# Kernel tuning notes

Hardware: AMD Instinct MI355X
Metric: run time of the kernel (lower is better)

Reference implementation:

```python
import jax, jax.numpy as jnp
import numpy as np

KS = 3        # kernel_size
DIL = 2       # dilation
HEAD_DIM = 32


def _unfold(x, ks, dil):
    """torch nn.Unfold(ks, dilation=dil, padding=dil*(ks-1)//2, stride=1).
    x: [B, C, H, W] -> [B, C, ks*ks, H, W] (channel-major patch order, matching torch)."""
    B, C, H, W = x.shape
    pad = dil * (ks - 1) // 2
    xp = jnp.pad(x, ((0, 0), (0, 0), (pad, pad), (pad, pad)))
    pats = [xp[:, :, i * dil:i * dil + H, j * dil:j * dil + W]
            for i in range(ks) for j in range(ks)]
    return jnp.stack(pats, axis=2)


def setup_inputs() -> dict:
    key = jax.random.key(0)
    k1, k2, k3 = jax.random.split(key, 3)
    shape = (16, 128, 64, 64)  # [B, d, H, W]
    return {
        "q": jax.random.normal(k1, shape, dtype=jnp.float32),
        "k": jax.random.normal(k2, shape, dtype=jnp.float32),
        "v": jax.random.normal(k3, shape, dtype=jnp.float32),
    }


def reference(q, k, v):
    B, d, H, W = q.shape
    heads = d // HEAD_DIM
    scale = HEAD_DIM ** (-0.5)
    KK = KS * KS
    # q: [B, heads, head_dim, H*W]
    qr = q.reshape(B, heads, HEAD_DIM, H * W)
    # unfolded k/v: [B, heads, head_dim, KK, H*W]
    ku = _unfold(k, KS, DIL).reshape(B, heads, HEAD_DIM, KK, H * W)
    vu = _unfold(v, KS, DIL).reshape(B, heads, HEAD_DIM, KK, H * W)
    # per-pixel small attention over KK local dilated keys
    attn = jnp.einsum('bhdn,bhdkn->bhnk', qr, ku) * scale  # [B,heads,HW,KK]
    attn = jax.nn.softmax(attn, axis=-1)  # attn_drop = 0 -> identity
    out = jnp.einsum('bhnk,bhdkn->bnhd', attn, vu)  # [B,HW,heads,head_dim]
    return out.reshape(B, H, W, d)
```

## Files before the change

### kernel.cpp

```cpp
#include <hip/hip_runtime.h>

namespace {
constexpr float SCALE = 0.17677669529663687f;
constexpr int CHP = 256;

typedef const __attribute__((address_space(1))) void gbl_v;
typedef __attribute__((address_space(3))) void lds_v;
typedef float v2f __attribute__((ext_vector_type(2)));

__global__ __launch_bounds__(512, 4) void dilate_attn(
    const float* __restrict__ q, const float* __restrict__ k,
    const float* __restrict__ v, float* __restrict__ out) {
  __shared__ float kbuf[32 * CHP];
  __shared__ float vbuf[32 * CHP];

  const int tid = threadIdx.x;
  const int cg  = tid & 7;
  const int pp  = (tid >> 3) & 31;
  const int rg  = tid >> 8;

  const int blk   = blockIdx.x;
  const int s     = blk >> 3;
  const int combo = ((blk & 7) << 3) | (s >> 5);
  const int pr    = s & 31;
  const int r0    = ((pr >> 1) << 2) | (pr & 1);
  const int b     = combo >> 2;
  const int head  = combo & 3;
  const int qrow  = r0 + 2 * rg;

  const size_t cb = ((size_t)b * 128 + head * 32) * 4096;
  const float* kp = k + cb;
  const float* vp = v + cb;

  int srow[4]; float vm[4];
  #pragma unroll
  for (int j = 0; j < 4; ++j) {
    const int ry = r0 - 2 + 2 * j;
    const bool ok = (unsigned)ry < 64u;
    srow[j] = (ok ? ry : r0) * 64;
    vm[j]   = ok ? 1.0f : 0.0f;
  }

  const int px0 = pp << 1;
  v2f q2[4];
  #pragma unroll
  for (int ci = 0; ci < 4; ++ci) {
    q2[ci] = *(const v2f*)(q + cb + (cg * 4 + ci) * 4096 + qrow * 64 + px0);
    q2[ci] *= SCALE;
  }

  int goff[4], loff[4];
  #pragma unroll
  for (int t = 0; t < 4; ++t) {
    const int l4  = t * 512 + tid;
    const int ch  = l4 >> 6;
    const int rem = l4 & 63;
    const int r   = rem >> 4;
    const int q4  = rem & 15;
    const int pxs = ((q4 - (ch >> 2)) & 15) << 2;
    goff[t] = ch * 4096 + srow[r] + pxs;
    loff[t] = l4 << 2;
  }
  #pragma unroll
  for (int t = 0; t < 4; ++t)
    __builtin_amdgcn_global_load_lds((gbl_v*)(kp + goff[t]), (lds_v*)(kbuf + loff[t]), 16, 0, 0);
  #pragma unroll
  for (int t = 0; t < 4; ++t)
    __builtin_amdgcn_global_load_lds((gbl_v*)(vp + goff[t]), (lds_v*)(vbuf + loff[t]), 16, 0, 0);

  asm volatile("s_waitcnt vmcnt(4)" ::: "memory");
  __builtin_amdgcn_s_barrier();
  asm volatile("" ::: "memory");

  const int   txL = (pp == 0)  ? 0  : px0 - 2;
  const int   txC = px0;
  const int   txR = (pp == 31) ? 62 : px0 + 2;
  const float mL  = (pp == 0)  ? 0.0f : 1.0f;
  const float mR  = (pp == 31) ? 0.0f : 1.0f;

  const int rot = cg << 2;
  const int tL  = (txL + rot) & 63;
  const int tC  = (txC + rot) & 63;
  const int tR  = (txR + rot) & 63;

  const int rbase = rg;

  v2f l[9];
  #pragma unroll
  for (int t = 0; t < 9; ++t) l[t] = (v2f)(0.0f);

  #pragma unroll
  for (int r = 0; r < 3; ++r) {
    #pragma unroll
    for (int ci = 0; ci < 4; ++ci) {
      const float* kc = kbuf + (cg * 4 + ci) * CHP + (rbase + r) * 64;
      const v2f kL = *(const v2f*)(kc + tL);
      const v2f kC = *(const v2f*)(kc + tC);
      const v2f kR = *(const v2f*)(kc + tR);
      l[r*3+0] = __builtin_elementwise_fma(q2[ci], kL, l[r*3+0]);
      l[r*3+1] = __builtin_elementwise_fma(q2[ci], kC, l[r*3+1]);
      l[r*3+2] = __builtin_elementwise_fma(q2[ci], kR, l[r*3+2]);
    }
  }

  #pragma unroll
  for (int m = 1; m <= 4; m <<= 1) {
    #pragma unroll
    for (int t = 0; t < 9; ++t) {
      v2f tmp;
      tmp.x = __shfl_xor(l[t].x, m, 64);
      tmp.y = __shfl_xor(l[t].y, m, 64);
      l[t] += tmp;
    }
  }

  float msk[9];
  #pragma unroll
  for (int r = 0; r < 3; ++r) {
    msk[r*3+0] = vm[rbase + r] * mL;
    msk[r*3+1] = vm[rbase + r];
    msk[r*3+2] = vm[rbase + r] * mR;
  }
  v2f sum = (v2f)(0.0f);
  #pragma unroll
  for (int t = 0; t < 9; ++t) {
    l[t] *= msk[t];
    l[t].x = __expf(l[t].x);
    l[t].y = __expf(l[t].y);
    sum += l[t];
  }
  v2f rv; rv.x = 1.0f / sum.x; rv.y = 1.0f / sum.y;
  #pragma unroll
  for (int t = 0; t < 9; ++t)
    l[t] *= rv * msk[t];

  asm volatile("s_waitcnt vmcnt(0)" ::: "memory");
  __builtin_amdgcn_s_barrier();
  asm volatile("" ::: "memory");

  v2f o[4];
  #pragma unroll
  for (int ci = 0; ci < 4; ++ci) o[ci] = (v2f)(0.0f);
  #pragma unroll
  for (int r = 0; r < 3; ++r) {
    #pragma unroll
    for (int ci = 0; ci < 4; ++ci) {
      const float* vc = vbuf + (cg * 4 + ci) * CHP + (rbase + r) * 64;
      const v2f vL = *(const v2f*)(vc + tL);
      const v2f vC = *(const v2f*)(vc + tC);
      const v2f vR = *(const v2f*)(vc + tR);
      o[ci] = __builtin_elementwise_fma(l[r*3+0], vL, o[ci]);
      o[ci] = __builtin_elementwise_fma(l[r*3+1], vC, o[ci]);
      o[ci] = __builtin_elementwise_fma(l[r*3+2], vR, o[ci]);
    }
  }

  float* ob = out + ((size_t)(b * 64 + qrow) * 64 + px0) * 128 + head * 32 + cg * 4;
  *(float4*)(ob)       = make_float4(o[0].x, o[1].x, o[2].x, o[3].x);
  *(float4*)(ob + 128) = make_float4(o[0].y, o[1].y, o[2].y, o[3].y);
}
}

extern "C" void kernel_launch(void* const* d_in, const int* in_sizes, int n_in,
                              void* d_out, int out_size, void* d_ws, size_t ws_size,
                              hipStream_t stream) {
  const float* q = (const float*)d_in[0];
  const float* k = (const float*)d_in[1];
  const float* v = (const float*)d_in[2];
  float* o = (float*)d_out;
  dilate_attn<<<dim3(2048), dim3(512), 0, stream>>>(q, k, v, o);
}
```

Before: 140.2 us.

## Share one LDS buffer for K then V and use DPP for reductions

Replaces the separate K and V LDS buffers with a single 32 KB buffer. K is loaded and consumed first, then V is loaded into the same space after a barrier, which halves LDS per block and raises the launch-bounds occupancy target from 4 to 8. The first two butterfly steps of the channel reduction now use quad-permute DPP moves instead of ds_bpermute shuffles. In exchange, the V load no longer overlaps the QK and softmax computation and is fully serialized, and the extra __syncthreads calls add barrier overhead.

```diff
diff --git a/kernel.cpp b/kernel.cpp
--- a/kernel.cpp
+++ b/kernel.cpp
@@ -8,11 +8,16 @@
 typedef __attribute__((address_space(3))) void lds_v;
 typedef float v2f __attribute__((ext_vector_type(2)));
 
-__global__ __launch_bounds__(512, 4) void dilate_attn(
+template<int CTRL>
+__device__ __forceinline__ float qperm(float v) {
+  return __builtin_bit_cast(float, __builtin_amdgcn_mov_dpp(
+      __builtin_bit_cast(int, v), CTRL, 0xF, 0xF, true));
+}
+
+__global__ __launch_bounds__(512, 8) void dilate_attn(
     const float* __restrict__ q, const float* __restrict__ k,
     const float* __restrict__ v, float* __restrict__ out) {
-  __shared__ float kbuf[32 * CHP];
-  __shared__ float vbuf[32 * CHP];
+  __shared__ float sbuf[32 * CHP];
 
   const int tid = threadIdx.x;
   const int cg  = tid & 7;
@@ -61,16 +66,11 @@
     goff[t] = ch * 4096 + srow[r] + pxs;
     loff[t] = l4 << 2;
   }
+
   #pragma unroll
   for (int t = 0; t < 4; ++t)
-    __builtin_amdgcn_global_load_lds((gbl_v*)(kp + goff[t]), (lds_v*)(kbuf + loff[t]), 16, 0, 0);
-  #pragma unroll
-  for (int t = 0; t < 4; ++t)
-    __builtin_amdgcn_global_load_lds((gbl_v*)(vp + goff[t]), (lds_v*)(vbuf + loff[t]), 16, 0, 0);
-
-  asm volatile("s_waitcnt vmcnt(4)" ::: "memory");
-  __builtin_amdgcn_s_barrier();
-  asm volatile("" ::: "memory");
+    __builtin_amdgcn_global_load_lds((gbl_v*)(kp + goff[t]), (lds_v*)(sbuf + loff[t]), 16, 0, 0);
+  __syncthreads();
 
   const int   txL = (pp == 0)  ? 0  : px0 - 2;
   const int   txC = px0;
@@ -93,7 +93,7 @@
   for (int r = 0; r < 3; ++r) {
     #pragma unroll
     for (int ci = 0; ci < 4; ++ci) {
-      const float* kc = kbuf + (cg * 4 + ci) * CHP + (rbase + r) * 64;
+      const float* kc = sbuf + (cg * 4 + ci) * CHP + (rbase + r) * 64;
       const v2f kL = *(const v2f*)(kc + tL);
       const v2f kC = *(const v2f*)(kc + tC);
       const v2f kR = *(const v2f*)(kc + tR);
@@ -104,14 +104,19 @@
   }
 
   #pragma unroll
-  for (int m = 1; m <= 4; m <<= 1) {
-    #pragma unroll
-    for (int t = 0; t < 9; ++t) {
-      v2f tmp;
-      tmp.x = __shfl_xor(l[t].x, m, 64);
-      tmp.y = __shfl_xor(l[t].y, m, 64);
-      l[t] += tmp;
-    }
+  for (int t = 0; t < 9; ++t) {
+    l[t].x += qperm<0xB1>(l[t].x);
+    l[t].y += qperm<0xB1>(l[t].y);
+  }
+  #pragma unroll
+  for (int t = 0; t < 9; ++t) {
+    l[t].x += qperm<0x4E>(l[t].x);
+    l[t].y += qperm<0x4E>(l[t].y);
+  }
+  #pragma unroll
+  for (int t = 0; t < 9; ++t) {
+    l[t].x += __shfl_xor(l[t].x, 4, 64);
+    l[t].y += __shfl_xor(l[t].y, 4, 64);
   }
 
   float msk[9];
@@ -134,9 +139,11 @@
   for (int t = 0; t < 9; ++t)
     l[t] *= rv * msk[t];
 
-  asm volatile("s_waitcnt vmcnt(0)" ::: "memory");
-  __builtin_amdgcn_s_barrier();
-  asm volatile("" ::: "memory");
+  __syncthreads();
+  #pragma unroll
+  for (int t = 0; t < 4; ++t)
+    __builtin_amdgcn_global_load_lds((gbl_v*)(vp + goff[t]), (lds_v*)(sbuf + loff[t]), 16, 0, 0);
+  __syncthreads();
 
   v2f o[4];
   #pragma unroll
@@ -145,7 +152,7 @@
   for (int r = 0; r < 3; ++r) {
     #pragma unroll
     for (int ci = 0; ci < 4; ++ci) {
-      const float* vc = vbuf + (cg * 4 + ci) * CHP + (rbase + r) * 64;
+      const float* vc = sbuf + (cg * 4 + ci) * CHP + (rbase + r) * 64;
       const v2f vL = *(const v2f*)(vc + tL);
       const v2f vC = *(const v2f*)(vc + tC);
       const v2f vR = *(const v2f*)(vc + tR);
```

After: 142.2 us. About the same (+1.4%).
